# Performance work log

Hardware: AMD Instinct MI355X
Metric: run time of the kernel (lower is better)

## Reference

```python
import jax, jax.numpy as jnp
import numpy as np

N = 100000          # total nodes
F = 128             # in_features
B = 1000            # number of graphs
NPG = 100           # nodes per graph (contiguous)
DEG = 16            # avg degree
E = B * NPG * DEG   # total edges (intra-graph)
K_RATIO = 0.8
KNUM = max(1, int(K_RATIO * NPG))  # nodes kept per graph = 80


def setup_inputs() -> dict:
    key = jax.random.key(0)
    k1, k2, k3, k4 = jax.random.split(key, 4)
    x = jax.random.normal(k1, (N, F), dtype=jnp.float32)
    # intra-graph random edges: offset each block of NPG*DEG edges by its graph's base node id
    offs = (jnp.arange(E, dtype=jnp.int32) // (NPG * DEG)) * NPG
    src = jax.random.randint(k2, (E,), 0, NPG, dtype=jnp.int32) + offs
    dst = jax.random.randint(k3, (E,), 0, NPG, dtype=jnp.int32) + offs
    edge_index = jnp.stack([src, dst], axis=0)
    batch = (jnp.arange(N, dtype=jnp.int32) // NPG).astype(jnp.int32)
    limit = float(np.sqrt(6.0 / (F + 1)))  # xavier_uniform for (F,1)
    theta_att = jax.random.uniform(k4, (F, 1), dtype=jnp.float32, minval=-limit, maxval=limit)
    return {"x": x, "edge_index": edge_index, "batch": batch, "theta_att": theta_att}


def reference(x, edge_index, batch, theta_att):
    num_nodes = x.shape[0]
    # add self loops with weight 1
    loops = jnp.arange(num_nodes, dtype=edge_index.dtype)
    row = jnp.concatenate([edge_index[0], loops])
    col = jnp.concatenate([edge_index[1], loops])
    w = jnp.ones(row.shape[0], dtype=x.dtype)
    # symmetric degree normalization (degree counted over row, as in torch code)
    deg = jax.ops.segment_sum(w, row, num_segments=num_nodes)
    dis = jnp.where(deg > 0, jax.lax.rsqrt(deg), jnp.zeros((), x.dtype))
    norm = dis[row] * w * dis[col]
    # scatter-add: agg[dst] += x[src] * norm
    agg = jax.ops.segment_sum(x[row] * norm[:, None], col, num_segments=num_nodes)
    z = (agg @ theta_att)[:, 0]                     # (N,)
    # per-graph top-k: graphs are contiguous and equal-sized -> reshape
    zb = z.reshape(B, NPG)
    _, pos = jax.lax.top_k(zb, KNUM)                # (B, KNUM) positions within each graph
    pos = jnp.sort(pos, axis=1)                     # global sort of keep_idx == per-graph sort here
    keep = (pos + jnp.arange(B, dtype=pos.dtype)[:, None] * NPG).reshape(-1)  # (B*KNUM,)
    scale = jax.nn.sigmoid(z[keep])[:, None]
    x_new = x[keep] * scale                         # (B*KNUM, F)
    batch_new = batch[keep]
    # subgraph with relabeled nodes; dropped edges padded with -1 (fixed shape for jit)
    node_mask = jnp.zeros(num_nodes, dtype=bool).at[keep].set(True)
    new_id = jnp.cumsum(node_mask.astype(jnp.int32)) - 1
    emask = node_mask[edge_index[0]] & node_mask[edge_index[1]]
    edge_index_new = jnp.where(emask[None, :], new_id[edge_index], -1)
    return x_new, edge_index_new, batch_new
```

## Files before the change

### kernel.cpp

```cpp
#include <hip/hip_runtime.h>


#define NPG   100
#define EPG   1600
#define KNUM  80
#define FDIM  128

__global__ __launch_bounds__(256)
void sagpool_fused(const float* __restrict__ x,
                   const int*   __restrict__ ei,
                   const float* __restrict__ theta,
                   float* __restrict__ out,
                   int E_total, int out_x_elems)
{
    const int g    = blockIdx.x;
    const int tid  = threadIdx.x;
    const int wave = tid >> 6;
    const int lane = tid & 63;
    const int base = g * NPG;

    __shared__ float  sh_theta[FDIM];
    __shared__ int    sh_src[EPG];
    __shared__ int    sh_dst[EPG];
    __shared__ int    sh_deg[NPG];
    __shared__ double sh_dis[NPG];
    __shared__ double sh_s[NPG];
    __shared__ double sh_z[NPG];
    __shared__ int    sh_kept[NPG];
    __shared__ int    sh_newid[NPG];
    __shared__ int    sh_keepnode[KNUM];
    __shared__ float  sh_scale[KNUM];

    if (tid < FDIM) sh_theta[tid] = theta[tid];
    if (tid < NPG)  sh_deg[tid] = 1;
    __syncthreads();

    for (int j = tid; j < EPG; j += 256) {
        int s = ei[g * EPG + j]           - base;
        int d = ei[E_total + g * EPG + j] - base;
        sh_src[j] = s;
        sh_dst[j] = d;
        atomicAdd(&sh_deg[s], 1);
    }
    __syncthreads();

    if (tid < NPG) sh_dis[tid] = 1.0 / sqrt((double)sh_deg[tid]);

    const double th0 = (double)sh_theta[2 * lane];
    const double th1 = (double)sh_theta[2 * lane + 1];
    for (int n = wave; n < NPG; n += 4) {
        float2 xv = ((const float2*)(x + (size_t)(base + n) * FDIM))[lane];
        double p = (double)xv.x * th0 + (double)xv.y * th1;
        #pragma unroll
        for (int off = 32; off > 0; off >>= 1)
            p += __shfl_down(p, off, 64);
        if (lane == 0) sh_s[n] = p;
    }
    __syncthreads();

    if (tid < NPG) sh_z[tid] = sh_s[tid] * sh_dis[tid] * sh_dis[tid];
    __syncthreads();

    for (int j = tid; j < EPG; j += 256) {
        int s = sh_src[j], d = sh_dst[j];
        atomicAdd(&sh_z[d], sh_s[s] * sh_dis[s] * sh_dis[d]);
    }
    __syncthreads();

    if (tid < NPG) {
        double zi = sh_z[tid];
        int rank = 0;
        for (int j = 0; j < NPG; ++j) {
            double zj = sh_z[j];
            rank += (int)((zj > zi) | ((zj == zi) & (j < tid)));
        }
        sh_kept[tid] = (rank < KNUM) ? 1 : 0;
    }
    __syncthreads();

    if (tid < NPG) {
        int r = 0;
        for (int j = 0; j < tid; ++j) r += sh_kept[j];
        if (sh_kept[tid]) {
            int row = g * KNUM + r;
            sh_newid[tid]  = row;
            sh_keepnode[r] = tid;
            sh_scale[r]    = (float)(1.0 / (1.0 + exp(-sh_z[tid])));
            out[(size_t)out_x_elems + 2 * (size_t)E_total + row] = (float)g;
        } else {
            sh_newid[tid] = -1;
        }
    }
    __syncthreads();

    for (int r = wave; r < KNUM; r += 4) {
        int   node = base + sh_keepnode[r];
        float sc   = sh_scale[r];
        float2 xv  = ((const float2*)(x + (size_t)node * FDIM))[lane];
        float2 o;
        o.x = xv.x * sc;
        o.y = xv.y * sc;
        ((float2*)(out + (size_t)(g * KNUM + r) * FDIM))[lane] = o;
    }

    float* out_e0 = out + out_x_elems;
    float* out_e1 = out_e0 + E_total;
    for (int j = tid; j < EPG; j += 256) {
        int a = sh_newid[sh_src[j]];
        int b = sh_newid[sh_dst[j]];
        bool valid = (a >= 0) && (b >= 0);
        out_e0[g * EPG + j] = valid ? (float)a : -1.0f;
        out_e1[g * EPG + j] = valid ? (float)b : -1.0f;
    }
}

extern "C" void kernel_launch(void* const* d_in, const int* in_sizes, int n_in,
                              void* d_out, int out_size, void* d_ws, size_t ws_size,
                              hipStream_t stream)
{
    const float* x     = (const float*)d_in[0];
    const int*   ei    = (const int*)d_in[1];
    const float* theta = (const float*)d_in[3];
    float* out = (float*)d_out;

    const int N = in_sizes[0] / FDIM;
    const int E = in_sizes[1] / 2;
    const int B = N / NPG;
    const int out_x_elems = B * KNUM * FDIM;

    sagpool_fused<<<dim3(B), dim3(256), 0, stream>>>(x, ei, theta, out, E, out_x_elems);
}
```

Baseline: 133.6 us.

## Split fused per-graph kernel into dot, topology, and gather kernels

The single per-graph kernel is split into three launches. A wide kernel computes the per-node x·theta dot products, a per-graph kernel does degree normalization, top-k, and edge relabeling, and a wide kernel gathers and scales the kept rows. The aim is to spread the bandwidth-heavy x reads over many small blocks instead of 1000 blocks with serialized phases. The cost is two extra launches, a workspace round trip for scores, keep indices and scales, and reading the kept x rows a second time.

```diff
diff --git a/kernel.cpp b/kernel.cpp
--- a/kernel.cpp
+++ b/kernel.cpp
@@ -7,19 +7,31 @@
 #define FDIM  128
 
 __global__ __launch_bounds__(256)
-void sagpool_fused(const float* __restrict__ x,
-                   const int*   __restrict__ ei,
-                   const float* __restrict__ theta,
-                   float* __restrict__ out,
-                   int E_total, int out_x_elems)
+void k_dot(const float* __restrict__ x, const float* __restrict__ theta,
+           double* __restrict__ s, int N)
+{
+    const int lane = threadIdx.x & 63;
+    const int node = (blockIdx.x * 256 + threadIdx.x) >> 6;
+    if (node >= N) return;
+    const double th0 = (double)theta[2 * lane];
+    const double th1 = (double)theta[2 * lane + 1];
+    float2 xv = ((const float2*)(x + (size_t)node * FDIM))[lane];
+    double p = (double)xv.x * th0 + (double)xv.y * th1;
+    #pragma unroll
+    for (int off = 32; off > 0; off >>= 1)
+        p += __shfl_down(p, off, 64);
+    if (lane == 0) s[node] = p;
+}
+
+__global__ __launch_bounds__(256)
+void k_topo(const int* __restrict__ ei, const double* __restrict__ s_g,
+            float* __restrict__ out, int E_total, int out_x_elems,
+            int* __restrict__ keep, float* __restrict__ scale)
 {
     const int g    = blockIdx.x;
     const int tid  = threadIdx.x;
-    const int wave = tid >> 6;
-    const int lane = tid & 63;
     const int base = g * NPG;
 
-    __shared__ float  sh_theta[FDIM];
     __shared__ int    sh_src[EPG];
     __shared__ int    sh_dst[EPG];
     __shared__ int    sh_deg[NPG];
@@ -28,11 +40,11 @@
     __shared__ double sh_z[NPG];
     __shared__ int    sh_kept[NPG];
     __shared__ int    sh_newid[NPG];
-    __shared__ int    sh_keepnode[KNUM];
-    __shared__ float  sh_scale[KNUM];
 
-    if (tid < FDIM) sh_theta[tid] = theta[tid];
-    if (tid < NPG)  sh_deg[tid] = 1;
+    if (tid < NPG) {
+        sh_deg[tid] = 1;
+        sh_s[tid]   = s_g[base + tid];
+    }
     __syncthreads();
 
     for (int j = tid; j < EPG; j += 256) {
@@ -45,17 +57,6 @@
     __syncthreads();
 
     if (tid < NPG) sh_dis[tid] = 1.0 / sqrt((double)sh_deg[tid]);
-
-    const double th0 = (double)sh_theta[2 * lane];
-    const double th1 = (double)sh_theta[2 * lane + 1];
-    for (int n = wave; n < NPG; n += 4) {
-        float2 xv = ((const float2*)(x + (size_t)(base + n) * FDIM))[lane];
-        double p = (double)xv.x * th0 + (double)xv.y * th1;
-        #pragma unroll
-        for (int off = 32; off > 0; off >>= 1)
-            p += __shfl_down(p, off, 64);
-        if (lane == 0) sh_s[n] = p;
-    }
     __syncthreads();
 
     if (tid < NPG) sh_z[tid] = sh_s[tid] * sh_dis[tid] * sh_dis[tid];
@@ -83,25 +84,15 @@
         for (int j = 0; j < tid; ++j) r += sh_kept[j];
         if (sh_kept[tid]) {
             int row = g * KNUM + r;
-            sh_newid[tid]  = row;
-            sh_keepnode[r] = tid;
-            sh_scale[r]    = (float)(1.0 / (1.0 + exp(-sh_z[tid])));
+            sh_newid[tid] = row;
+            keep[row]  = base + tid;
+            scale[row] = (float)(1.0 / (1.0 + exp(-sh_z[tid])));
             out[(size_t)out_x_elems + 2 * (size_t)E_total + row] = (float)g;
         } else {
             sh_newid[tid] = -1;
         }
     }
     __syncthreads();
-
-    for (int r = wave; r < KNUM; r += 4) {
-        int   node = base + sh_keepnode[r];
-        float sc   = sh_scale[r];
-        float2 xv  = ((const float2*)(x + (size_t)node * FDIM))[lane];
-        float2 o;
-        o.x = xv.x * sc;
-        o.y = xv.y * sc;
-        ((float2*)(out + (size_t)(g * KNUM + r) * FDIM))[lane] = o;
-    }
 
     float* out_e0 = out + out_x_elems;
     float* out_e1 = out_e0 + E_total;
@@ -112,6 +103,22 @@
         out_e0[g * EPG + j] = valid ? (float)a : -1.0f;
         out_e1[g * EPG + j] = valid ? (float)b : -1.0f;
     }
+}
+
+__global__ __launch_bounds__(256)
+void k_gather(const float* __restrict__ x, const int* __restrict__ keep,
+              const float* __restrict__ scale, float* __restrict__ out, int rows)
+{
+    const int lane = threadIdx.x & 63;
+    const int row  = (blockIdx.x * 256 + threadIdx.x) >> 6;
+    if (row >= rows) return;
+    const int   node = keep[row];
+    const float sc   = scale[row];
+    float2 xv = ((const float2*)(x + (size_t)node * FDIM))[lane];
+    float2 o;
+    o.x = xv.x * sc;
+    o.y = xv.y * sc;
+    ((float2*)(out + (size_t)row * FDIM))[lane] = o;
 }
 
 extern "C" void kernel_launch(void* const* d_in, const int* in_sizes, int n_in,
@@ -127,6 +134,13 @@
     const int E = in_sizes[1] / 2;
     const int B = N / NPG;
     const int out_x_elems = B * KNUM * FDIM;
+    const int rows = B * KNUM;
 
-    sagpool_fused<<<dim3(B), dim3(256), 0, stream>>>(x, ei, theta, out, E, out_x_elems);
+    double* s_ws   = (double*)d_ws;
+    int*    keep   = (int*)(s_ws + N);
+    float*  scale  = (float*)(keep + rows);
+
+    k_dot<<<dim3((N * 64 + 255) / 256), dim3(256), 0, stream>>>(x, theta, s_ws, N);
+    k_topo<<<dim3(B), dim3(256), 0, stream>>>(ei, s_ws, out, E, out_x_elems, keep, scale);
+    k_gather<<<dim3((rows * 64 + 255) / 256), dim3(256), 0, stream>>>(x, keep, scale, out, rows);
 }
```

New measurement: 142.8 us. 6.9% more time.
